# Optimization experiments

Measured on AMD Instinct MI355X. Metric: run time of the kernel, lower is better.

## Reference

```python
import jax, jax.numpy as jnp
import numpy as np

N_NODES = 50000
N_EDGES = 1000000
F = 64


def setup_inputs() -> dict:
    key = jax.random.key(0)
    k1, k2, k3, k4, k5 = jax.random.split(key, 5)
    nodes = jax.random.normal(k1, (N_NODES, F), dtype=jnp.float32)
    edges = jax.random.normal(k2, (N_EDGES, F), dtype=jnp.float32)
    edge_index = jax.random.randint(k3, (2, N_EDGES), 0, N_NODES, dtype=jnp.int64)
    edge_pairs = jax.random.randint(k4, (1, N_EDGES), 0, N_EDGES, dtype=jnp.int64)
    return {"nodes": nodes, "edges": edges, "edge_index": edge_index, "edge_pairs": edge_pairs}


def reference(nodes, edges, edge_index, edge_pairs):
    # AggregateLocalEdges(scatter_sum): sum edge messages into receiving node (edge_index[0])
    pooled = jax.ops.segment_sum(edges, edge_index[0], num_segments=nodes.shape[0])  # [N, F]
    # GatherNodesOutgoing: gather pooled node features back onto edges at edge_index[1]
    ed_new = pooled[edge_index[1]]  # [M, F]
    # GatherEdgesPairs: gather reverse-edge message
    ed_not = edges[edge_pairs[0]]  # [M, F]
    # Subtract
    return ed_new - ed_not
```

## Files before the change

kernel.cpp:

```cpp
#include <hip/hip_runtime.h>
#include <hip/hip_fp16.h>

#define FDIM 64
#define BLK 256

typedef float f32x4 __attribute__((ext_vector_type(4)));

__global__ void dmpnn_scatter_h2(const float4* __restrict__ edges4,
                                 const int* __restrict__ recv,
                                 __half2* __restrict__ pooled,
                                 long long total ) {
    long long tid = (long long)blockIdx.x * blockDim.x + threadIdx.x;
    if (tid >= total) return;
    int e = (int)(tid >> 4);
    int g = (int)(tid & 15);
    float4 v = edges4[tid];
    int node = recv[e];
    __half2* dst = &pooled[((long long)node << 5) + (g << 1)];
    unsafeAtomicAdd(dst + 0, __floats2half2_rn(v.x, v.y));
    unsafeAtomicAdd(dst + 1, __floats2half2_rn(v.z, v.w));
}

__global__ void dmpnn_gather_sub(const __half2* __restrict__ pooled,
                                 const float4* __restrict__ edges4,
                                 const int* __restrict__ send,
                                 const int* __restrict__ pair,
                                 float4* __restrict__ out4,
                                 long long total ) {
    long long tid = (long long)blockIdx.x * blockDim.x + threadIdx.x;
    if (tid >= total) return;
    int e = (int)(tid >> 4);
    int q = (int)(tid & 15);
    int sn = send[e];
    int pe = pair[e];
    const __half2* ph = &pooled[((long long)sn << 5) + (q << 1)];
    __half2 h0 = ph[0];
    __half2 h1 = ph[1];
    float2 a0 = __half22float2(h0);
    float2 a1 = __half22float2(h1);
    float4 b = edges4[(long long)pe * 16 + q];
    f32x4 r;
    r.x = a0.x - b.x;
    r.y = a0.y - b.y;
    r.z = a1.x - b.z;
    r.w = a1.y - b.w;
    __builtin_nontemporal_store(r, (f32x4*)&out4[tid]);
}

__global__ void dmpnn_scatter_add(const float* __restrict__ edges,
                                  const int* __restrict__ recv,
                                  float* __restrict__ pooled,
                                  long long total) {
    long long tid = (long long)blockIdx.x * blockDim.x + threadIdx.x;
    if (tid >= total) return;
    int e = (int)(tid >> 6);
    int f = (int)(tid & 63);
    atomicAdd(&pooled[(long long)recv[e] * FDIM + f], edges[tid]);
}

__global__ void dmpnn_gather_sub_f32(const float4* __restrict__ pooled4,
                                     const float4* __restrict__ edges4,
                                     const int* __restrict__ send,
                                     const int* __restrict__ pair,
                                     float4* __restrict__ out4,
                                     long long total) {
    long long tid = (long long)blockIdx.x * blockDim.x + threadIdx.x;
    if (tid >= total) return;
    int e = (int)(tid >> 4);
    int q = (int)(tid & 15);
    float4 a = pooled4[(long long)send[e] * 16 + q];
    float4 b = edges4[(long long)pair[e] * 16 + q];
    f32x4 r;
    r.x = a.x - b.x; r.y = a.y - b.y; r.z = a.z - b.z; r.w = a.w - b.w;
    __builtin_nontemporal_store(r, (f32x4*)&out4[tid]);
}

extern "C" void kernel_launch(void* const* d_in, const int* in_sizes, int n_in,
                              void* d_out, int out_size, void* d_ws, size_t ws_size,
                              hipStream_t stream) {
    const float* edges      = (const float*)d_in[1];
    const int*   edge_index = (const int*)d_in[2];
    const int*   edge_pairs = (const int*)d_in[3];

    const int N = in_sizes[0] / FDIM;
    const int M = in_sizes[1] / FDIM;

    const int* recv = edge_index;
    const int* send = edge_index + M;

    size_t need_h = (size_t)N * FDIM * sizeof(__half);

    long long total16 = (long long)M * 16;
    unsigned grid16 = (unsigned)((total16 + BLK - 1) / BLK);

    if (ws_size >= need_h) {
        __half2* pooled = (__half2*)d_ws;

        (void)hipMemsetAsync(pooled, 0, need_h, stream);

        dmpnn_scatter_h2<<<dim3(grid16), dim3(BLK), 0, stream>>>(
            (const float4*)edges, recv, pooled, total16);

        dmpnn_gather_sub<<<dim3(grid16), dim3(BLK), 0, stream>>>(
            pooled, (const float4*)edges, send, edge_pairs,
            (float4*)d_out, total16);
    } else {
        float* pooled = (float*)d_ws;
        (void)hipMemsetAsync(pooled, 0, (size_t)N * FDIM * sizeof(float), stream);
        long long totalS = (long long)M * FDIM;
        dmpnn_scatter_add<<<dim3((unsigned)((totalS + BLK - 1) / BLK)), dim3(BLK), 0, stream>>>(
            edges, recv, pooled, totalS);
        dmpnn_gather_sub_f32<<<dim3(grid16), dim3(BLK), 0, stream>>>(
            (const float4*)pooled, (const float4*)edges, send, edge_pairs,
            (float4*)d_out, total16);
    }
}
```

Measured before the change: 298.3 us.

## Privatize scatter accumulators per XCD with fp32 workgroup-scope atomics, then reduce

Measured after the change: 987.0 us. +230.8%, slower.

```diff
diff --git a/kernel.cpp b/kernel.cpp
--- a/kernel.cpp
+++ b/kernel.cpp
@@ -3,13 +3,67 @@
 
 #define FDIM 64
 #define BLK 256
+#define NCOPY 8
 
 typedef float f32x4 __attribute__((ext_vector_type(4)));
+
+__global__ void dmpnn_scatter_xcd(const float4* __restrict__ edges4,
+                                  const int* __restrict__ recv,
+                                  float* __restrict__ copies,
+                                  long long total ,
+                                  long long cstride ) {
+    long long tid = (long long)blockIdx.x * blockDim.x + threadIdx.x;
+    if (tid >= total) return;
+    int e = (int)(tid >> 4);
+    int q = (int)(tid & 15);
+    float4 v = edges4[tid];
+    int node = recv[e];
+    unsigned xcc;
+    asm volatile("s_getreg_b32 %0, hwreg(HW_REG_XCC_ID)" : "=s"(xcc));
+    float* dst = copies + (size_t)(xcc & (NCOPY - 1)) * cstride
+               + ((size_t)node << 6) + (q << 2);
+    __hip_atomic_fetch_add(dst + 0, v.x, __ATOMIC_RELAXED, __HIP_MEMORY_SCOPE_WORKGROUP);
+    __hip_atomic_fetch_add(dst + 1, v.y, __ATOMIC_RELAXED, __HIP_MEMORY_SCOPE_WORKGROUP);
+    __hip_atomic_fetch_add(dst + 2, v.z, __ATOMIC_RELAXED, __HIP_MEMORY_SCOPE_WORKGROUP);
+    __hip_atomic_fetch_add(dst + 3, v.w, __ATOMIC_RELAXED, __HIP_MEMORY_SCOPE_WORKGROUP);
+}
+
+__global__ void dmpnn_reduce(const float* __restrict__ copies,
+                             float4* __restrict__ pooled4,
+                             int totalQ ,
+                             long long cstrideQ ) {
+    int t = blockIdx.x * blockDim.x + threadIdx.x;
+    if (t >= totalQ) return;
+    const f32x4* c4 = (const f32x4*)copies;
+    f32x4 acc = __builtin_nontemporal_load(&c4[t]);
+    #pragma unroll
+    for (int c = 1; c < NCOPY; ++c)
+        acc += __builtin_nontemporal_load(&c4[(long long)c * cstrideQ + t]);
+    float4 r; r.x = acc.x; r.y = acc.y; r.z = acc.z; r.w = acc.w;
+    pooled4[t] = r;
+}
+
+__global__ void dmpnn_gather_sub_f32(const float4* __restrict__ pooled4,
+                                     const float4* __restrict__ edges4,
+                                     const int* __restrict__ send,
+                                     const int* __restrict__ pair,
+                                     float4* __restrict__ out4,
+                                     long long total ) {
+    long long tid = (long long)blockIdx.x * blockDim.x + threadIdx.x;
+    if (tid >= total) return;
+    int e = (int)(tid >> 4);
+    int q = (int)(tid & 15);
+    float4 a = pooled4[(long long)send[e] * 16 + q];
+    float4 b = edges4[(long long)pair[e] * 16 + q];
+    f32x4 r;
+    r.x = a.x - b.x; r.y = a.y - b.y; r.z = a.z - b.z; r.w = a.w - b.w;
+    __builtin_nontemporal_store(r, (f32x4*)&out4[tid]);
+}
 
 __global__ void dmpnn_scatter_h2(const float4* __restrict__ edges4,
                                  const int* __restrict__ recv,
                                  __half2* __restrict__ pooled,
-                                 long long total ) {
+                                 long long total) {
     long long tid = (long long)blockIdx.x * blockDim.x + threadIdx.x;
     if (tid >= total) return;
     int e = (int)(tid >> 4);
@@ -21,57 +75,22 @@
     unsafeAtomicAdd(dst + 1, __floats2half2_rn(v.z, v.w));
 }
 
-__global__ void dmpnn_gather_sub(const __half2* __restrict__ pooled,
-                                 const float4* __restrict__ edges4,
-                                 const int* __restrict__ send,
-                                 const int* __restrict__ pair,
-                                 float4* __restrict__ out4,
-                                 long long total ) {
+__global__ void dmpnn_gather_sub_h2(const __half2* __restrict__ pooled,
+                                    const float4* __restrict__ edges4,
+                                    const int* __restrict__ send,
+                                    const int* __restrict__ pair,
+                                    float4* __restrict__ out4,
+                                    long long total) {
     long long tid = (long long)blockIdx.x * blockDim.x + threadIdx.x;
     if (tid >= total) return;
     int e = (int)(tid >> 4);
     int q = (int)(tid & 15);
-    int sn = send[e];
-    int pe = pair[e];
-    const __half2* ph = &pooled[((long long)sn << 5) + (q << 1)];
-    __half2 h0 = ph[0];
-    __half2 h1 = ph[1];
-    float2 a0 = __half22float2(h0);
-    float2 a1 = __half22float2(h1);
-    float4 b = edges4[(long long)pe * 16 + q];
-    f32x4 r;
-    r.x = a0.x - b.x;
-    r.y = a0.y - b.y;
-    r.z = a1.x - b.z;
-    r.w = a1.y - b.w;
-    __builtin_nontemporal_store(r, (f32x4*)&out4[tid]);
-}
-
-__global__ void dmpnn_scatter_add(const float* __restrict__ edges,
-                                  const int* __restrict__ recv,
-                                  float* __restrict__ pooled,
-                                  long long total) {
-    long long tid = (long long)blockIdx.x * blockDim.x + threadIdx.x;
-    if (tid >= total) return;
-    int e = (int)(tid >> 6);
-    int f = (int)(tid & 63);
-    atomicAdd(&pooled[(long long)recv[e] * FDIM + f], edges[tid]);
-}
-
-__global__ void dmpnn_gather_sub_f32(const float4* __restrict__ pooled4,
-                                     const float4* __restrict__ edges4,
-                                     const int* __restrict__ send,
-                                     const int* __restrict__ pair,
-                                     float4* __restrict__ out4,
-                                     long long total) {
-    long long tid = (long long)blockIdx.x * blockDim.x + threadIdx.x;
-    if (tid >= total) return;
-    int e = (int)(tid >> 4);
-    int q = (int)(tid & 15);
-    float4 a = pooled4[(long long)send[e] * 16 + q];
+    const __half2* ph = &pooled[((long long)send[e] << 5) + (q << 1)];
+    float2 a0 = __half22float2(ph[0]);
+    float2 a1 = __half22float2(ph[1]);
     float4 b = edges4[(long long)pair[e] * 16 + q];
     f32x4 r;
-    r.x = a.x - b.x; r.y = a.y - b.y; r.z = a.z - b.z; r.w = a.w - b.w;
+    r.x = a0.x - b.x; r.y = a0.y - b.y; r.z = a1.x - b.z; r.w = a1.y - b.w;
     __builtin_nontemporal_store(r, (f32x4*)&out4[tid]);
 }
 
@@ -88,30 +107,36 @@
     const int* recv = edge_index;
     const int* send = edge_index + M;
 
-    size_t need_h = (size_t)N * FDIM * sizeof(__half);
+    long long cstride  = (long long)N * FDIM;
+    long long total16  = (long long)M * 16;
+    unsigned  grid16   = (unsigned)((total16 + BLK - 1) / BLK);
+    int       totalQ   = N * 16;
+    unsigned  gridQ    = (unsigned)((totalQ + BLK - 1) / BLK);
 
-    long long total16 = (long long)M * 16;
-    unsigned grid16 = (unsigned)((total16 + BLK - 1) / BLK);
+    size_t need = ((size_t)NCOPY + 1) * (size_t)cstride * sizeof(float);
 
-    if (ws_size >= need_h) {
-        __half2* pooled = (__half2*)d_ws;
+    if (ws_size >= need) {
+        float* copies = (float*)d_ws;
+        float* pooled = copies + (size_t)NCOPY * cstride;
 
-        (void)hipMemsetAsync(pooled, 0, need_h, stream);
+        (void)hipMemsetAsync(copies, 0, (size_t)NCOPY * cstride * sizeof(float), stream);
 
-        dmpnn_scatter_h2<<<dim3(grid16), dim3(BLK), 0, stream>>>(
-            (const float4*)edges, recv, pooled, total16);
+        dmpnn_scatter_xcd<<<dim3(grid16), dim3(BLK), 0, stream>>>(
+            (const float4*)edges, recv, copies, total16, cstride);
 
-        dmpnn_gather_sub<<<dim3(grid16), dim3(BLK), 0, stream>>>(
-            pooled, (const float4*)edges, send, edge_pairs,
-            (float4*)d_out, total16);
-    } else {
-        float* pooled = (float*)d_ws;
-        (void)hipMemsetAsync(pooled, 0, (size_t)N * FDIM * sizeof(float), stream);
-        long long totalS = (long long)M * FDIM;
-        dmpnn_scatter_add<<<dim3((unsigned)((totalS + BLK - 1) / BLK)), dim3(BLK), 0, stream>>>(
-            edges, recv, pooled, totalS);
+        dmpnn_reduce<<<dim3(gridQ), dim3(BLK), 0, stream>>>(
+            copies, (float4*)pooled, totalQ, cstride / 4);
+
         dmpnn_gather_sub_f32<<<dim3(grid16), dim3(BLK), 0, stream>>>(
             (const float4*)pooled, (const float4*)edges, send, edge_pairs,
             (float4*)d_out, total16);
+    } else {
+        __half2* pooled = (__half2*)d_ws;
+        (void)hipMemsetAsync(pooled, 0, (size_t)N * FDIM * sizeof(__half), stream);
+        dmpnn_scatter_h2<<<dim3(grid16), dim3(BLK), 0, stream>>>(
+            (const float4*)edges, recv, pooled, total16);
+        dmpnn_gather_sub_h2<<<dim3(grid16), dim3(BLK), 0, stream>>>(
+            pooled, (const float4*)edges, send, edge_pairs,
+            (float4*)d_out, total16);
     }
 }
```
